# Performance work log

Hardware: AMD Instinct MI355X
Metric: run time of the kernel (lower is better)

## Reference

```python
import jax, jax.numpy as jnp
import numpy as np

B, PS, ENC = 64, 14, 2048
DEC, ATT, EMB = 512, 512, 512
V, L = 10000, 52


def setup_inputs() -> dict:
    key = jax.random.key(0)
    ks = jax.random.split(key, 24)
    rn = lambda k, shp, s=0.02: (jax.random.normal(k, shp) * s).astype(jnp.float32)
    lengths = jax.random.randint(ks[2], (B, 1), 2, L + 1)
    lengths = lengths.at[0, 0].set(L)  # ensure max(decode_lengths) == L-1 (static)
    return {
        "encoder_output": jax.random.normal(ks[0], (B, PS, PS, ENC), jnp.float32),
        "encoded_captions": jax.random.randint(ks[1], (B, L), 0, V),
        "caption_lengths": lengths,
        # embedding (torch init: uniform(-0.1, 0.1))
        "emb_W": jax.random.uniform(ks[3], (V, EMB), jnp.float32, -0.1, 0.1),
        # attention linears
        "att_enc_W": rn(ks[4], (ENC, ATT)), "att_enc_b": jnp.zeros((ATT,), jnp.float32),
        "att_dec_W": rn(ks[5], (DEC, ATT)), "att_dec_b": jnp.zeros((ATT,), jnp.float32),
        "att_full_w": rn(ks[6], (ATT,)), "att_full_b": jnp.zeros((), jnp.float32),
        # LSTMCell(input = EMB + ENC, hidden = DEC)
        "lstm_Wih": rn(ks[7], (4 * DEC, EMB + ENC)), "lstm_Whh": rn(ks[8], (4 * DEC, DEC)),
        "lstm_bih": jnp.zeros((4 * DEC,), jnp.float32), "lstm_bhh": jnp.zeros((4 * DEC,), jnp.float32),
        # init_h / init_c / f_beta / fc
        "initH_W": rn(ks[9], (ENC, DEC)), "initH_b": jnp.zeros((DEC,), jnp.float32),
        "initC_W": rn(ks[10], (ENC, DEC)), "initC_b": jnp.zeros((DEC,), jnp.float32),
        "fbeta_W": rn(ks[11], (DEC, ENC)), "fbeta_b": jnp.zeros((ENC,), jnp.float32),
        "fc_W": jax.random.uniform(ks[12], (DEC, V), jnp.float32, -0.1, 0.1),
        "fc_b": jnp.zeros((V,), jnp.float32),
    }


def reference(encoder_output, encoded_captions, caption_lengths,
              emb_W, att_enc_W, att_enc_b, att_dec_W, att_dec_b,
              att_full_w, att_full_b, lstm_Wih, lstm_Whh, lstm_bih, lstm_bhh,
              initH_W, initH_b, initC_W, initC_b, fbeta_W, fbeta_b, fc_W, fc_b):
    b = encoder_output.shape[0]
    lengths = caption_lengths[:, 0]
    order = jnp.argsort(-lengths)                     # sort descending (sort_idx)
    lengths = lengths[order]
    enc = encoder_output.reshape(b, -1, ENC)[order]   # [B, P, ENC]
    caps = encoded_captions[order]                    # [B, L]
    emb = emb_W[caps]                                 # [B, L, EMB]
    dec_len = lengths - 1                             # decode lengths
    T = caps.shape[1] - 1                             # static max(decode_lengths)

    mean_enc = enc.mean(axis=1)
    h0 = mean_enc @ initH_W + initH_b
    c0 = mean_enc @ initC_W + initC_b
    # precompute encoder half of the attention MLP once
    att1 = jnp.einsum('bpe,ea->bpa', enc, att_enc_W) + att_enc_b  # [B, P, ATT]

    def step(carry, t):
        h, c = carry
        mask = (t < dec_len)[:, None]                 # rows still decoding
        att2 = h @ att_dec_W + att_dec_b              # [B, ATT]
        e = jax.nn.relu(att1 + att2[:, None, :]) @ att_full_w + att_full_b  # [B, P]
        alpha = jax.nn.softmax(e, axis=-1)
        awe = jnp.einsum('bp,bpe->be', alpha, enc)    # attention-weighted encoding
        gate = jax.nn.sigmoid(h @ fbeta_W + fbeta_b)
        x = jnp.concatenate([emb[:, t, :], gate * awe], axis=1)
        gates = x @ lstm_Wih.T + lstm_bih + h @ lstm_Whh.T + lstm_bhh
        i, f, g, o = jnp.split(gates, 4, axis=1)
        c_new = jax.nn.sigmoid(f) * c + jax.nn.sigmoid(i) * jnp.tanh(g)
        h_new = jax.nn.sigmoid(o) * jnp.tanh(c_new)
        pred = h_new @ fc_W + fc_b                    # dropout p=0 -> identity
        h = jnp.where(mask, h_new, h)
        c = jnp.where(mask, c_new, c)
        return (h, c), (jnp.where(mask, pred, 0.0), jnp.where(mask, alpha, 0.0))

    _, (preds, alphas) = jax.lax.scan(step, (h0, c0), jnp.arange(T))
    preds = jnp.transpose(preds, (1, 0, 2))           # [B, T, V]
    alphas = jnp.transpose(alphas, (1, 0, 2))         # [B, T, P]
    return preds, caps, dec_len, alphas, order
```

## Files before the change

kernel.cpp:

```cpp
#include <hip/hip_runtime.h>
#include <hip/hip_cooperative_groups.h>
#include <math.h>

namespace cg = cooperative_groups;

#define BATCH 64
#define PIX   196
#define ENCD  2048
#define DECD  512
#define ATTD  512
#define EMBD  512
#define VOC   10000
#define LCAP  52
#define TSTEPS 51
#define XHDIM 3072

typedef __bf16 bfv8 __attribute__((ext_vector_type(8)));
typedef float  fv4  __attribute__((ext_vector_type(4)));

__device__ __forceinline__ float bf2f(unsigned short u) {
    union { unsigned int i; float f; } x; x.i = ((unsigned int)u) << 16; return x.f;
}
__device__ __forceinline__ unsigned short f2bf(float f) {
    union { float f; unsigned int i; } x; x.f = f;
    unsigned int r = x.i + 0x7fffu + ((x.i >> 16) & 1u);
    return (unsigned short)(r >> 16);
}

__global__ void k_setup(const int* caps, const int* lens,
                        int* order, int* declen,
                        float* caps_out, float* declen_out, float* order_out) {
    __shared__ int sl[64];
    __shared__ int so[64];
    int tid = threadIdx.x;
    sl[tid] = lens[tid];
    __syncthreads();
    int li = sl[tid];
    int pos = 0;
    for (int j = 0; j < 64; ++j) {
        int lj = sl[j];
        if (lj > li || (lj == li && j < tid)) pos++;
    }
    so[pos] = tid;
    __syncthreads();
    int ob = so[tid];
    order[tid] = ob;
    int dl = sl[ob] - 1;
    declen[tid] = dl;
    order_out[tid] = (float)ob;
    declen_out[tid] = (float)dl;
    for (int l = 0; l < LCAP; ++l)
        caps_out[tid * LCAP + l] = (float)caps[ob * LCAP + l];
}

__global__ void k_emb_all(const float* embW, const int* caps, const int* order,
                          unsigned short* emb_all, unsigned short* xh) {
    int b = blockIdx.x, t = blockIdx.y, tid = threadIdx.x;
    int tok = caps[order[b] * LCAP + t];
    float4 v = *(const float4*)(embW + (size_t)tok * EMBD + tid * 4);
    ushort4 o;
    o.x = f2bf(v.x); o.y = f2bf(v.y); o.z = f2bf(v.z); o.w = f2bf(v.w);
    *(ushort4*)(emb_all + ((size_t)t * 64 + b) * EMBD + tid * 4) = o;
    if (t == 0)
        *(ushort4*)(xh + (size_t)b * XHDIM + tid * 4) = o;
}

__global__ __launch_bounds__(256) void k_cvt_T(const float* src, unsigned short* dst,
                                               int R, int C) {
    __shared__ float tile[64][65];
    int c0 = blockIdx.x * 64, r0 = blockIdx.y * 64, tid = threadIdx.x;
    for (int idx = tid; idx < 4096; idx += 256) {
        int r = idx >> 6, c = idx & 63;
        float v = 0.f;
        if (r0 + r < R && c0 + c < C) v = src[(size_t)(r0 + r) * C + c0 + c];
        tile[r][c] = v;
    }
    __syncthreads();
    for (int idx = tid; idx < 4096; idx += 256) {
        int c = idx >> 6, r = idx & 63;
        if (c0 + c < C && r0 + r < R)
            dst[(size_t)(c0 + c) * R + r0 + r] = f2bf(tile[r][c]);
    }
}

__global__ void k_cvt_comb(const float* Wih, const float* Whh, unsigned short* W) {
    int j = blockIdx.x, tid = threadIdx.x;
    int q = j >> 9, d = j & 511;
    int nr = ((d >> 4) << 6) + (q << 4) + (d & 15);
    for (int k = tid * 4; k < XHDIM; k += 1024) {
        const float* src = (k < 2560) ? (Wih + (size_t)j * 2560 + k)
                                      : (Whh + (size_t)j * 512 + (k - 2560));
        float4 v = *(const float4*)src;
        ushort4 o;
        o.x = f2bf(v.x); o.y = f2bf(v.y); o.z = f2bf(v.z); o.w = f2bf(v.w);
        *(ushort4*)(W + (size_t)nr * XHDIM + k) = o;
    }
}

__global__ void k_cvt_enc(const float* enc, const int* order, unsigned short* enc_bf) {
    int b = blockIdx.x, p = blockIdx.y, tid = threadIdx.x;
    const float* src = enc + ((size_t)order[b] * PIX + p) * ENCD + tid * 8;
    float4 v0 = *(const float4*)src;
    float4 v1 = *(const float4*)(src + 4);
    unsigned short o[8];
    o[0] = f2bf(v0.x); o[1] = f2bf(v0.y); o[2] = f2bf(v0.z); o[3] = f2bf(v0.w);
    o[4] = f2bf(v1.x); o[5] = f2bf(v1.y); o[6] = f2bf(v1.z); o[7] = f2bf(v1.w);
    *(uint4*)(enc_bf + ((size_t)b * PIX + p) * ENCD + tid * 8) = *(uint4*)o;
}

__global__ void k_mean(const float* enc, const int* order, float* meanv) {
    int b = blockIdx.x;
    int col = blockIdx.y * 256 + threadIdx.x;
    int ob = order[b];
    const float* base = enc + (size_t)ob * PIX * ENCD + col;
    float acc = 0.f;
    for (int p = 0; p < PIX; ++p) acc += base[(size_t)p * ENCD];
    meanv[b * ENCD + col] = acc * (1.0f / (float)PIX);
}

__global__ __launch_bounds__(256) void k_h0c0(const float* meanv,
                                              const float* WH, const float* bH,
                                              const float* WC, const float* bC,
                                              float* h, float* c, unsigned short* xh) {
    __shared__ float As[64 * 33];
    __shared__ float Bs[32 * 65];
    int nt = blockIdx.x, tid = threadIdx.x;
    const float* W; const float* bias; float* out; int j0; bool isH;
    if (nt < 8) { W = WH; bias = bH; out = h; j0 = nt * 64; isH = true; }
    else        { W = WC; bias = bC; out = c; j0 = (nt - 8) * 64; isH = false; }
    float acc[4][4] = {};
    int tr = tid & 15, tc = tid >> 4;
    for (int k0 = 0; k0 < ENCD; k0 += 32) {
        for (int idx = tid; idx < 512; idx += 256) {
            int rl = idx >> 3, k4 = (idx & 7) << 2;
            float4 v = *(const float4*)(meanv + (size_t)rl * ENCD + k0 + k4);
            float* d = As + rl * 33 + k4;
            d[0] = v.x; d[1] = v.y; d[2] = v.z; d[3] = v.w;
        }
        for (int idx = tid; idx < 512; idx += 256) {
            int k = idx >> 4, j4 = (idx & 15) << 2;
            float4 v = *(const float4*)(W + (size_t)(k0 + k) * DECD + j0 + j4);
            float* d = Bs + k * 65 + j4;
            d[0] = v.x; d[1] = v.y; d[2] = v.z; d[3] = v.w;
        }
        __syncthreads();
        for (int kk = 0; kk < 32; ++kk) {
            float a[4], bb[4];
            for (int i = 0; i < 4; ++i) a[i] = As[(tr * 4 + i) * 33 + kk];
            for (int i = 0; i < 4; ++i) bb[i] = Bs[kk * 65 + tc * 4 + i];
            for (int i = 0; i < 4; ++i)
                for (int j2 = 0; j2 < 4; ++j2) acc[i][j2] += a[i] * bb[j2];
        }
        __syncthreads();
    }
    for (int i = 0; i < 4; ++i)
        for (int j2 = 0; j2 < 4; ++j2) {
            int r = tr * 4 + i, j = j0 + tc * 4 + j2;
            float v = acc[i][j2] + bias[j];
            out[r * DECD + j] = v;
            if (isH) xh[(size_t)r * XHDIM + 2560 + j] = f2bf(v);
        }
}

__device__ __forceinline__ void mm64_core(
    const unsigned short* __restrict__ A, int lda,
    const unsigned short* __restrict__ Bt, int ldb,
    int K, int nvalid,
    unsigned short* __restrict__ As, unsigned short* __restrict__ Bs,
    fv4* __restrict__ acc)
{
    const int tid = threadIdx.x;
    const int lane = tid & 63;
    const int w = tid >> 6, wr = w >> 1, wc = w & 1;
    const int lr = lane & 15, lk = (lane >> 4) << 3;
    const int sr = tid >> 2, sc = (tid & 3) << 3;
    const unsigned short* ap = A + (size_t)sr * lda + sc;
    const unsigned short* bp = Bt + (size_t)sr * ldb + sc;
    const bool bok = sr < nvalid;
    unsigned short* aw = As + sr * 40 + sc;
    unsigned short* bw = Bs + sr * 40 + sc;
    const unsigned short* a0p = As + (wr * 32 + lr) * 40 + lk;
    const unsigned short* a1p = a0p + 16 * 40;
    const unsigned short* b0p = Bs + (wc * 32 + lr) * 40 + lk;
    const unsigned short* b1p = b0p + 16 * 40;

    uint4 av = *(const uint4*)ap;
    uint4 bv;
    if (bok) bv = *(const uint4*)bp; else { bv.x = bv.y = bv.z = bv.w = 0u; }

    for (int k0 = 0; k0 < K; k0 += 32) {
        __syncthreads();
        *(uint4*)aw = av;
        *(uint4*)bw = bv;
        if (k0 + 32 < K) {
            av = *(const uint4*)(ap + k0 + 32);
            if (bok) bv = *(const uint4*)(bp + k0 + 32);
            else { bv.x = bv.y = bv.z = bv.w = 0u; }
        }
        __syncthreads();
        bfv8 a0 = *(const bfv8*)a0p;
        bfv8 a1 = *(const bfv8*)a1p;
        bfv8 b0 = *(const bfv8*)b0p;
        bfv8 b1 = *(const bfv8*)b1p;
        acc[0] = __builtin_amdgcn_mfma_f32_16x16x32_bf16(a0, b0, acc[0], 0, 0, 0);
        acc[1] = __builtin_amdgcn_mfma_f32_16x16x32_bf16(a0, b1, acc[1], 0, 0, 0);
        acc[2] = __builtin_amdgcn_mfma_f32_16x16x32_bf16(a1, b0, acc[2], 0, 0, 0);
        acc[3] = __builtin_amdgcn_mfma_f32_16x16x32_bf16(a1, b1, acc[3], 0, 0, 0);
    }
}

#define MM64_DECL_EPI \
    int lane = threadIdx.x & 63; int w = threadIdx.x >> 6; \
    int wr = w >> 1, wc = w & 1; \
    int rg = (lane >> 4) << 2, cg = lane & 15;

__global__ __launch_bounds__(256) void k_att1_mfma(
    const unsigned short* __restrict__ enc_bf, const unsigned short* __restrict__ WaeT,
    const float* __restrict__ bias, unsigned short* __restrict__ att1bf) {
    __shared__ __align__(16) unsigned short As[64 * 40];
    __shared__ __align__(16) unsigned short Bs[64 * 40];
    int r0 = blockIdx.x * 64, a0 = blockIdx.y * 64;
    fv4 acc[4];
    acc[0] = (fv4)0.f; acc[1] = (fv4)0.f; acc[2] = (fv4)0.f; acc[3] = (fv4)0.f;
    mm64_core(enc_bf + (size_t)r0 * ENCD, ENCD,
              WaeT + (size_t)a0 * ENCD, ENCD, ENCD, 64, As, Bs, acc);
    MM64_DECL_EPI
    #pragma unroll
    for (int m = 0; m < 2; ++m)
      #pragma unroll
      for (int n = 0; n < 2; ++n)
        #pragma unroll
        for (int r = 0; r < 4; ++r) {
            int row = r0 + wr * 32 + m * 16 + rg + r;
            int col = a0 + wc * 32 + n * 16 + cg;
            att1bf[(size_t)row * ATTD + col] = f2bf(acc[m * 2 + n][r] + bias[col]);
        }
}

__device__ __forceinline__ void fc_tile(
    const unsigned short* __restrict__ hallbf, const unsigned short* __restrict__ WfcT,
    const float* __restrict__ bias, const int* __restrict__ declen,
    float* __restrict__ preds, int vt, int tt,
    unsigned short* __restrict__ As, unsigned short* __restrict__ Bs) {
    int v0 = vt * 64;
    int nv = VOC - v0; if (nv > 64) nv = 64;
    fv4 acc[4];
    acc[0] = (fv4)0.f; acc[1] = (fv4)0.f; acc[2] = (fv4)0.f; acc[3] = (fv4)0.f;
    mm64_core(hallbf + (size_t)tt * 64 * DECD, DECD,
              WfcT + (size_t)v0 * DECD, DECD, DECD, nv, As, Bs, acc);
    MM64_DECL_EPI
    #pragma unroll
    for (int m = 0; m < 2; ++m)
      #pragma unroll
      for (int n = 0; n < 2; ++n)
        #pragma unroll
        for (int r = 0; r < 4; ++r) {
            int b = wr * 32 + m * 16 + rg + r;
            int v = v0 + wc * 32 + n * 16 + cg;
            if (v < VOC) {
                bool mask = tt < declen[b];
                preds[((size_t)b * TSTEPS + tt) * VOC + v] =
                    mask ? (acc[m * 2 + n][r] + bias[v]) : 0.f;
            }
        }
}

__global__ __launch_bounds__(256) void k_fc_mfma(
    const unsigned short* __restrict__ hallbf, const unsigned short* __restrict__ WfcT,
    const float* __restrict__ bias, const int* __restrict__ declen,
    float* __restrict__ preds) {
    __shared__ __align__(16) unsigned short As[64 * 40];
    __shared__ __align__(16) unsigned short Bs[64 * 40];
    fc_tile(hallbf, WfcT, bias, declen, preds, blockIdx.x, blockIdx.y, As, Bs);
}

struct LoopArgs {
    const unsigned short* W2T;
    const unsigned short* Wcomb;
    const unsigned short* att1;
    const unsigned short* enc;
    const unsigned short* emb_all;
    const unsigned short* WfcT;
    unsigned short* xh;
    unsigned short* hall;
    const float* bad; const float* bfb;
    const float* wfull; const float* bfull;
    const float* bih; const float* bhh;
    const float* fcb;
    float* att2; float* gate; float* part5;
    float* h; float* c; float* alphas; float* preds;
    const int* declen;
};

__global__ __launch_bounds__(256) void k_loop(LoopArgs a) {
    cg::grid_group grid = cg::this_grid();
    __shared__ __align__(16) unsigned short As[64 * 40];
    __shared__ __align__(16) unsigned short Bs[64 * 40];
    __shared__ float sal[256];
    __shared__ float sred[256];
    __shared__ float sacc[2048];
    __shared__ float gacc[64][65];
    const int bid = blockIdx.x, tid = threadIdx.x;

    for (int t = 0; t < TSTEPS; ++t) {
        if (bid < 40) {
            int j0 = bid * 64;
            fv4 acc[4];
            acc[0] = (fv4)0.f; acc[1] = (fv4)0.f; acc[2] = (fv4)0.f; acc[3] = (fv4)0.f;
            mm64_core(a.xh + 2560, XHDIM, a.W2T + (size_t)j0 * DECD, DECD,
                      DECD, 64, As, Bs, acc);
            MM64_DECL_EPI
            #pragma unroll
            for (int m = 0; m < 2; ++m)
              #pragma unroll
              for (int n = 0; n < 2; ++n)
                #pragma unroll
                for (int r = 0; r < 4; ++r) {
                    int row = wr * 32 + m * 16 + rg + r;
                    int jg = j0 + wc * 32 + n * 16 + cg;
                    float v = acc[m * 2 + n][r];
                    if (jg < ATTD) {
                        a.att2[row * ATTD + jg] = v + a.bad[jg];
                    } else {
                        int jj = jg - ATTD;
                        a.gate[row * ENCD + jj] = 1.f / (1.f + expf(-(v + a.bfb[jj])));
                    }
                }
        } else if (bid < 72) {
            int jt = bid - 40;
            fv4 acc[4];
            acc[0] = (fv4)0.f; acc[1] = (fv4)0.f; acc[2] = (fv4)0.f; acc[3] = (fv4)0.f;
            mm64_core(a.xh + 2560, XHDIM,
                      a.Wcomb + (size_t)jt * 64 * XHDIM + 2560, XHDIM,
                      512, 64, As, Bs, acc);
            MM64_DECL_EPI
            #pragma unroll
            for (int m = 0; m < 2; ++m)
              #pragma unroll
              for (int n = 0; n < 2; ++n)
                #pragma unroll
                for (int r = 0; r < 4; ++r) {
                    int row = wr * 32 + m * 16 + rg + r;
                    int col = jt * 64 + wc * 32 + n * 16 + cg;
                    a.part5[row * 2048 + col] = acc[m * 2 + n][r];
                }
        }
        grid.sync();

        {
            int b = bid >> 2, pair = bid & 3;
            int lane = tid & 63, wv = tid >> 6;
            const float* a2 = a.att2 + b * ATTD + lane * 8;
            float4 a2a = *(const float4*)a2;
            float4 a2b = *(const float4*)(a2 + 4);
            const float* wf = a.wfull + lane * 8;
            float4 wfa = *(const float4*)wf;
            float4 wfb = *(const float4*)(wf + 4);
            float bf0 = a.bfull[0];
            for (int p = wv; p < PIX; p += 4) {
                uint4 v = *(const uint4*)(a.att1 + ((size_t)b * PIX + p) * ATTD + lane * 8);
                const unsigned short* us = (const unsigned short*)&v;
                float accv;
                accv  = fmaxf(bf2f(us[0]) + a2a.x, 0.f) * wfa.x;
                accv += fmaxf(bf2f(us[1]) + a2a.y, 0.f) * wfa.y;
                accv += fmaxf(bf2f(us[2]) + a2a.z, 0.f) * wfa.z;
                accv += fmaxf(bf2f(us[3]) + a2a.w, 0.f) * wfa.w;
                accv += fmaxf(bf2f(us[4]) + a2b.x, 0.f) * wfb.x;
                accv += fmaxf(bf2f(us[5]) + a2b.y, 0.f) * wfb.y;
                accv += fmaxf(bf2f(us[6]) + a2b.z, 0.f) * wfb.z;
                accv += fmaxf(bf2f(us[7]) + a2b.w, 0.f) * wfb.w;
                for (int off = 32; off; off >>= 1) accv += __shfl_down(accv, off);
                if (lane == 0) sacc[p] = accv + bf0;
            }
            __syncthreads();
            float ev = (tid < PIX) ? sacc[tid] : -1e30f;
            sred[tid] = ev; __syncthreads();
            for (int s = 128; s; s >>= 1) {
                if (tid < s) sred[tid] = fmaxf(sred[tid], sred[tid + s]);
                __syncthreads();
            }
            float m = sred[0]; __syncthreads();
            float pv = (tid < PIX) ? expf(ev - m) : 0.f;
            sred[tid] = pv; __syncthreads();
            for (int s = 128; s; s >>= 1) {
                if (tid < s) sred[tid] += sred[tid + s];
                __syncthreads();
            }
            float inv = 1.f / sred[0];
            float al = pv * inv;
            sal[tid] = al;
            if (pair == 0 && tid < PIX) {
                bool mask = t < a.declen[b];
                a.alphas[((size_t)b * TSTEPS + t) * PIX + tid] = mask ? al : 0.f;
            }
            if (tid < 16)
                *(uint4*)(a.xh + (size_t)b * XHDIM + pair * 128 + tid * 8) =
                    *(const uint4*)(a.emb_all + ((size_t)t * 64 + b) * EMBD +
                                    pair * 128 + tid * 8);
            __syncthreads();
            int g = tid & 31, pp = tid >> 5;
            #pragma unroll
            for (int cc = 0; cc < 2; ++cc) {
                int ch = pair * 2 + cc;
                float acc[8] = {};
                const unsigned short* base =
                    a.enc + (size_t)b * PIX * ENCD + ch * 256 + g * 8;
                for (int p = pp; p < PIX; p += 8) {
                    uint4 v = *(const uint4*)(base + (size_t)p * ENCD);
                    const unsigned short* us = (const unsigned short*)&v;
                    float av = sal[p];
                    #pragma unroll
                    for (int jj = 0; jj < 8; ++jj) acc[jj] += av * bf2f(us[jj]);
                }
                #pragma unroll
                for (int jj = 0; jj < 8; ++jj) sacc[pp * 256 + g * 8 + jj] = acc[jj];
                __syncthreads();
                float s = 0.f;
                #pragma unroll
                for (int q = 0; q < 8; ++q) s += sacc[q * 256 + tid];
                int col = ch * 256 + tid;
                a.xh[(size_t)b * XHDIM + EMBD + col] = f2bf(a.gate[b * ENCD + col] * s);
                __syncthreads();
            }
        }
        grid.sync();

        if (bid < 32) {
            int jt = bid;
            fv4 acc[4];
            acc[0] = (fv4)0.f; acc[1] = (fv4)0.f; acc[2] = (fv4)0.f; acc[3] = (fv4)0.f;
            mm64_core(a.xh, XHDIM, a.Wcomb + (size_t)jt * 64 * XHDIM, XHDIM,
                      2560, 64, As, Bs, acc);
            {
                MM64_DECL_EPI
                #pragma unroll
                for (int m = 0; m < 2; ++m)
                  #pragma unroll
                  for (int n = 0; n < 2; ++n)
                    #pragma unroll
                    for (int r = 0; r < 4; ++r)
                        gacc[wr * 32 + m * 16 + rg + r][wc * 32 + n * 16 + cg] =
                            acc[m * 2 + n][r];
            }
            __syncthreads();
            #pragma unroll
            for (int it = 0; it < 4; ++it) {
                int idx = it * 256 + tid;
                int b = idx >> 4, dd = idx & 15;
                int d = jt * 16 + dd;
                float gv[4];
                #pragma unroll
                for (int q = 0; q < 4; ++q) {
                    int ccol = q * 16 + dd;
                    gv[q] = gacc[b][ccol] + a.part5[b * 2048 + jt * 64 + ccol]
                          + a.bih[q * 512 + d] + a.bhh[q * 512 + d];
                }
                float si = 1.f / (1.f + expf(-gv[0]));
                float sf = 1.f / (1.f + expf(-gv[1]));
                float gg = tanhf(gv[2]);
                float so = 1.f / (1.f + expf(-gv[3]));
                float c_old = a.c[b * DECD + d], h_old = a.h[b * DECD + d];
                float c_new = sf * c_old + si * gg;
                float h_new = so * tanhf(c_new);
                bool mask = t < a.declen[b];
                float h_keep = mask ? h_new : h_old;
                a.h[b * DECD + d] = h_keep;
                a.c[b * DECD + d] = mask ? c_new : c_old;
                a.xh[(size_t)b * XHDIM + 2560 + d] = f2bf(h_keep);
                a.hall[((size_t)t * 64 + b) * DECD + d] = f2bf(h_new);
            }
        } else if (bid < 189) {
            if (t > 0)
                fc_tile(a.hall, a.WfcT, a.fcb, a.declen, a.preds,
                        bid - 32, t - 1, As, Bs);
        }
        grid.sync();
    }

    if (bid < 157)
        fc_tile(a.hall, a.WfcT, a.fcb, a.declen, a.preds, bid, TSTEPS - 1, As, Bs);
}

__global__ __launch_bounds__(256) void k_att2gate_mfma(
    const unsigned short* __restrict__ xh, const unsigned short* __restrict__ W2T,
    const float* __restrict__ bad, const float* __restrict__ bfb,
    float* __restrict__ att2, float* __restrict__ gate) {
    __shared__ __align__(16) unsigned short As[64 * 40];
    __shared__ __align__(16) unsigned short Bs[64 * 40];
    int j0 = blockIdx.x * 64;
    fv4 acc[4];
    acc[0] = (fv4)0.f; acc[1] = (fv4)0.f; acc[2] = (fv4)0.f; acc[3] = (fv4)0.f;
    mm64_core(xh + 2560, XHDIM, W2T + (size_t)j0 * DECD, DECD, DECD, 64, As, Bs, acc);
    MM64_DECL_EPI
    for (int m = 0; m < 2; ++m)
      for (int n = 0; n < 2; ++n)
        for (int r = 0; r < 4; ++r) {
            int row = wr * 32 + m * 16 + rg + r;
            int jg = j0 + wc * 32 + n * 16 + cg;
            float v = acc[m * 2 + n][r];
            if (jg < ATTD) att2[row * ATTD + jg] = v + bad[jg];
            else { int jj = jg - ATTD; gate[row * ENCD + jj] = 1.f / (1.f + expf(-(v + bfb[jj]))); }
        }
}

__global__ __launch_bounds__(256) void k_gates_mfma(
    const unsigned short* __restrict__ xh, const unsigned short* __restrict__ W,
    float* __restrict__ partial) {
    __shared__ __align__(16) unsigned short As[64 * 40];
    __shared__ __align__(16) unsigned short Bs[64 * 40];
    int jt = blockIdx.x, kc = blockIdx.y;
    fv4 acc[4];
    acc[0] = (fv4)0.f; acc[1] = (fv4)0.f; acc[2] = (fv4)0.f; acc[3] = (fv4)0.f;
    mm64_core(xh + kc * 512, XHDIM,
              W + (size_t)jt * 64 * XHDIM + kc * 512, XHDIM, 512, 64, As, Bs, acc);
    float* out = partial + (size_t)kc * (64 * 2048);
    MM64_DECL_EPI
    for (int m = 0; m < 2; ++m)
      for (int n = 0; n < 2; ++n)
        for (int r = 0; r < 4; ++r) {
            int row = wr * 32 + m * 16 + rg + r;
            int col = jt * 64 + wc * 32 + n * 16 + cg;
            out[row * 2048 + col] = acc[m * 2 + n][r];
        }
}

__global__ void k_e(const unsigned short* att1bf, const float* att2,
                    const float* wfull, const float* bfull, float* e) {
    __shared__ float a2s[512];
    __shared__ float wfs[512];
    int b = blockIdx.x, tid = threadIdx.x;
    a2s[tid] = att2[b * ATTD + tid];
    a2s[tid + 256] = att2[b * ATTD + tid + 256];
    wfs[tid] = wfull[tid];
    wfs[tid + 256] = wfull[tid + 256];
    __syncthreads();
    int p = blockIdx.y * 4 + (tid >> 6);
    int lane = tid & 63;
    uint4 v = *(const uint4*)(att1bf + ((size_t)b * PIX + p) * ATTD + lane * 8);
    const unsigned short* us = (const unsigned short*)&v;
    float acc = 0.f;
    for (int jj = 0; jj < 8; ++jj) {
        int a = lane * 8 + jj;
        float x = bf2f(us[jj]) + a2s[a];
        x = fmaxf(x, 0.f);
        acc += x * wfs[a];
    }
    for (int off = 32; off; off >>= 1) acc += __shfl_down(acc, off);
    if (lane == 0) e[b * PIX + p] = acc + bfull[0];
}

__global__ void k_awe(const float* e, const unsigned short* enc_bf,
                      const float* gate, const int* declen,
                      unsigned short* xh, float* alphas_out, int t) {
    __shared__ float sal[256];
    __shared__ float sred[256];
    __shared__ float sacc[2048];
    int b = blockIdx.x, ch = blockIdx.y, tid = threadIdx.x;
    float ev = (tid < PIX) ? e[b * PIX + tid] : -1e30f;
    sred[tid] = ev; __syncthreads();
    for (int s = 128; s; s >>= 1) { if (tid < s) sred[tid] = fmaxf(sred[tid], sred[tid + s]); __syncthreads(); }
    float m = sred[0]; __syncthreads();
    float pv = (tid < PIX) ? expf(ev - m) : 0.f;
    sred[tid] = pv; __syncthreads();
    for (int s = 128; s; s >>= 1) { if (tid < s) sred[tid] += sred[tid + s]; __syncthreads(); }
    float inv = 1.f / sred[0];
    float al = pv * inv;
    sal[tid] = al;
    if (ch == 0 && tid < PIX) {
        bool mask = t < declen[b];
        alphas_out[((size_t)b * TSTEPS + t) * PIX + tid] = mask ? al : 0.f;
    }
    __syncthreads();
    int g = tid & 31, pp = tid >> 5;
    float acc[8] = {};
    const unsigned short* base = enc_bf + (size_t)b * PIX * ENCD + ch * 256 + g * 8;
    for (int p = pp; p < PIX; p += 8) {
        uint4 v = *(const uint4*)(base + (size_t)p * ENCD);
        const unsigned short* us = (const unsigned short*)&v;
        float a = sal[p];
        for (int jj = 0; jj < 8; ++jj) acc[jj] += a * bf2f(us[jj]);
    }
    for (int jj = 0; jj < 8; ++jj) sacc[pp * 256 + g * 8 + jj] = acc[jj];
    __syncthreads();
    float s = 0.f;
    for (int q = 0; q < 8; ++q) s += sacc[q * 256 + tid];
    int col = ch * 256 + tid;
    xh[(size_t)b * XHDIM + EMBD + col] = f2bf(gate[b * ENCD + col] * s);
}

__global__ void k_update(const float* partial, const float* bih, const float* bhh,
                         const int* declen, float* h, float* c,
                         unsigned short* hallbf, const unsigned short* emb_all,
                         unsigned short* xh, int t) {
    int b = blockIdx.x, d = threadIdx.x;
    float g[4];
    for (int q = 0; q < 4; ++q) {
        int ncol = ((d >> 4) << 6) + (q << 4) + (d & 15);
        float acc = bih[q * 512 + d] + bhh[q * 512 + d];
        for (int kc = 0; kc < 6; ++kc) acc += partial[(size_t)kc * 131072 + b * 2048 + ncol];
        g[q] = acc;
    }
    float si = 1.f / (1.f + expf(-g[0]));
    float sf = 1.f / (1.f + expf(-g[1]));
    float gg = tanhf(g[2]);
    float so = 1.f / (1.f + expf(-g[3]));
    float c_old = c[b * DECD + d], h_old = h[b * DECD + d];
    float c_new = sf * c_old + si * gg;
    float h_new = so * tanhf(c_new);
    bool mask = t < declen[b];
    float h_keep = mask ? h_new : h_old;
    h[b * DECD + d] = h_keep;
    c[b * DECD + d] = mask ? c_new : c_old;
    xh[(size_t)b * XHDIM + 2560 + d] = f2bf(h_keep);
    hallbf[((size_t)t * 64 + b) * DECD + d] = f2bf(h_new);
    if (t + 1 < TSTEPS)
        xh[(size_t)b * XHDIM + d] = emb_all[((size_t)(t + 1) * 64 + b) * EMBD + d];
}

extern "C" void kernel_launch(void* const* d_in, const int* in_sizes, int n_in,
                              void* d_out, int out_size, void* d_ws, size_t ws_size,
                              hipStream_t stream) {
    const float* enc      = (const float*)d_in[0];
    const int*   caps     = (const int*)d_in[1];
    const int*   lens     = (const int*)d_in[2];
    const float* embW     = (const float*)d_in[3];
    const float* att_enc_W = (const float*)d_in[4];
    const float* att_enc_b = (const float*)d_in[5];
    const float* att_dec_W = (const float*)d_in[6];
    const float* att_dec_b = (const float*)d_in[7];
    const float* att_full_w = (const float*)d_in[8];
    const float* att_full_b = (const float*)d_in[9];
    const float* lstm_Wih = (const float*)d_in[10];
    const float* lstm_Whh = (const float*)d_in[11];
    const float* lstm_bih = (const float*)d_in[12];
    const float* lstm_bhh = (const float*)d_in[13];
    const float* initH_W  = (const float*)d_in[14];
    const float* initH_b  = (const float*)d_in[15];
    const float* initC_W  = (const float*)d_in[16];
    const float* initC_b  = (const float*)d_in[17];
    const float* fbeta_W  = (const float*)d_in[18];
    const float* fbeta_b  = (const float*)d_in[19];
    const float* fc_W     = (const float*)d_in[20];
    const float* fc_b     = (const float*)d_in[21];

    float* o = (float*)d_out;
    float* preds_out  = o;
    float* caps_out   = o + (size_t)BATCH * TSTEPS * VOC;
    float* declen_out = caps_out + (size_t)BATCH * LCAP;
    float* order_out  = declen_out + BATCH;
    float* alphas_out = order_out + BATCH;

    char* wsb = (char*)d_ws;
    int* i_order  = (int*)wsb;
    int* i_declen = i_order + 64;
    float* f = (float*)(wsb + 512);
    float* f_h     = f;  f += (size_t)BATCH * DECD;
    float* f_c     = f;  f += (size_t)BATCH * DECD;
    float* f_att2  = f;  f += (size_t)BATCH * ATTD;
    float* f_gate  = f;  f += (size_t)BATCH * ENCD;
    float* f_e     = f;  f += (size_t)BATCH * PIX;
    f = (float*)(((uintptr_t)f + 255) & ~(uintptr_t)255);
    float* f_part  = f;  f += (size_t)6 * BATCH * 2048;
    float* f_mean = f_part;
    unsigned short* WaeT = (unsigned short*)(f_part + (size_t)BATCH * ENCD);
    f = (float*)(((uintptr_t)f + 255) & ~(uintptr_t)255);
    unsigned short* bf = (unsigned short*)f;
    unsigned short* xh_bf    = bf;  bf += (size_t)BATCH * XHDIM;
    unsigned short* att1_bf  = bf;  bf += (size_t)BATCH * PIX * ATTD;
    unsigned short* Wcomb_bf = bf;  bf += (size_t)2048 * XHDIM;
    unsigned short* W2T      = bf;  bf += (size_t)(ATTD + ENCD) * DECD;
    unsigned short* WfcT     = bf;  bf += (size_t)VOC * DECD;
    unsigned short* emb_all  = bf;  bf += (size_t)TSTEPS * BATCH * EMBD;
    unsigned short* hall_bf  = bf;  bf += (size_t)TSTEPS * BATCH * DECD;
    bf = (unsigned short*)(((uintptr_t)bf + 255) & ~(uintptr_t)255);
    unsigned short* enc_bf   = bf;  bf += (size_t)BATCH * PIX * ENCD;

    k_setup<<<1, 64, 0, stream>>>(caps, lens, i_order, i_declen,
                                  caps_out, declen_out, order_out);
    k_emb_all<<<dim3(BATCH, TSTEPS), 128, 0, stream>>>(embW, caps, i_order,
                                                       emb_all, xh_bf);
    k_cvt_comb<<<2048, 256, 0, stream>>>(lstm_Wih, lstm_Whh, Wcomb_bf);
    k_cvt_enc<<<dim3(BATCH, PIX), 256, 0, stream>>>(enc, i_order, enc_bf);
    k_cvt_T<<<dim3(8, 8),   256, 0, stream>>>(att_dec_W, W2T, DECD, ATTD);
    k_cvt_T<<<dim3(32, 8),  256, 0, stream>>>(fbeta_W, W2T + (size_t)ATTD * DECD, DECD, ENCD);
    k_cvt_T<<<dim3(8, 32),  256, 0, stream>>>(att_enc_W, WaeT, ENCD, ATTD);
    k_cvt_T<<<dim3(157, 8), 256, 0, stream>>>(fc_W, WfcT, DECD, VOC);
    k_mean<<<dim3(BATCH, ENCD / 256), 256, 0, stream>>>(enc, i_order, f_mean);
    k_h0c0<<<16, 256, 0, stream>>>(f_mean, initH_W, initH_b, initC_W, initC_b,
                                   f_h, f_c, xh_bf);
    k_att1_mfma<<<dim3(PIX, ATTD / 64), 256, 0, stream>>>(enc_bf, WaeT,
                                                          att_enc_b, att1_bf);

    int maxb = 0;
    hipError_t qerr = hipOccupancyMaxActiveBlocksPerMultiprocessor(
        &maxb, (const void*)k_loop, 256, 0);
    bool coop_ok = (qerr == hipSuccess) && (maxb >= 1);

    if (coop_ok) {
        LoopArgs la;
        la.W2T = W2T; la.Wcomb = Wcomb_bf; la.att1 = att1_bf; la.enc = enc_bf;
        la.emb_all = emb_all; la.WfcT = WfcT; la.xh = xh_bf; la.hall = hall_bf;
        la.bad = att_dec_b; la.bfb = fbeta_b; la.wfull = att_full_w;
        la.bfull = att_full_b; la.bih = lstm_bih; la.bhh = lstm_bhh;
        la.fcb = fc_b;
        la.att2 = f_att2; la.gate = f_gate; la.part5 = f_part;
        la.h = f_h; la.c = f_c; la.alphas = alphas_out; la.preds = preds_out;
        la.declen = i_declen;
        void* kargs[] = { (void*)&la };
        hipError_t lerr = hipLaunchCooperativeKernel(
            (const void*)k_loop, dim3(256), dim3(256), kargs, 0, stream);
        coop_ok = (lerr == hipSuccess);
    }

    if (!coop_ok) {
        for (int t = 0; t < TSTEPS; ++t) {
            k_att2gate_mfma<<<40, 256, 0, stream>>>(xh_bf, W2T, att_dec_b, fbeta_b,
                                                    f_att2, f_gate);
            k_e<<<dim3(BATCH, 49), 256, 0, stream>>>(att1_bf, f_att2, att_full_w,
                                                     att_full_b, f_e);
            k_awe<<<dim3(BATCH, 8), 256, 0, stream>>>(f_e, enc_bf, f_gate, i_declen,
                                                      xh_bf, alphas_out, t);
            k_gates_mfma<<<dim3(32, 6), 256, 0, stream>>>(xh_bf, Wcomb_bf, f_part);
            k_update<<<BATCH, DECD, 0, stream>>>(f_part, lstm_bih, lstm_bhh, i_declen,
                                                 f_h, f_c, hall_bf, emb_all, xh_bf, t);
        }
        k_fc_mfma<<<dim3((VOC + 63) / 64, TSTEPS), 256, 0, stream>>>(hall_bf, WfcT,
                                                                     fc_b, i_declen,
                                                                     preds_out);
    }
}
```

Baseline: 2.708 ms.

## Rebalance cooperative decode loop work across grid and use MFMA for h0/c0 init

The persistent cooperative loop now uses grid-stride work distribution with up to 512 blocks. The fc projection tiles move into the first phase alongside the att2/gate and h-part GEMMs. The attention score computation is spread over all warps with a global e buffer, which adds an extra grid.sync per step. The softmax/awe stage uses one block per batch-row/octant instead of one per pair. Separately, the init_h/init_c GEMMs switch from an FP32 SIMT kernel to a bf16 MFMA kernel on transposed weights, which costs two extra conversion kernels and some precision.

```diff
diff --git a/kernel.cpp b/kernel.cpp
--- a/kernel.cpp
+++ b/kernel.cpp
@@ -108,58 +108,14 @@
     *(uint4*)(enc_bf + ((size_t)b * PIX + p) * ENCD + tid * 8) = *(uint4*)o;
 }
 
-__global__ void k_mean(const float* enc, const int* order, float* meanv) {
+__global__ void k_mean(const float* enc, const int* order, unsigned short* mean_bf) {
     int b = blockIdx.x;
     int col = blockIdx.y * 256 + threadIdx.x;
     int ob = order[b];
     const float* base = enc + (size_t)ob * PIX * ENCD + col;
     float acc = 0.f;
     for (int p = 0; p < PIX; ++p) acc += base[(size_t)p * ENCD];
-    meanv[b * ENCD + col] = acc * (1.0f / (float)PIX);
-}
-
-__global__ __launch_bounds__(256) void k_h0c0(const float* meanv,
-                                              const float* WH, const float* bH,
-                                              const float* WC, const float* bC,
-                                              float* h, float* c, unsigned short* xh) {
-    __shared__ float As[64 * 33];
-    __shared__ float Bs[32 * 65];
-    int nt = blockIdx.x, tid = threadIdx.x;
-    const float* W; const float* bias; float* out; int j0; bool isH;
-    if (nt < 8) { W = WH; bias = bH; out = h; j0 = nt * 64; isH = true; }
-    else        { W = WC; bias = bC; out = c; j0 = (nt - 8) * 64; isH = false; }
-    float acc[4][4] = {};
-    int tr = tid & 15, tc = tid >> 4;
-    for (int k0 = 0; k0 < ENCD; k0 += 32) {
-        for (int idx = tid; idx < 512; idx += 256) {
-            int rl = idx >> 3, k4 = (idx & 7) << 2;
-            float4 v = *(const float4*)(meanv + (size_t)rl * ENCD + k0 + k4);
-            float* d = As + rl * 33 + k4;
-            d[0] = v.x; d[1] = v.y; d[2] = v.z; d[3] = v.w;
-        }
-        for (int idx = tid; idx < 512; idx += 256) {
-            int k = idx >> 4, j4 = (idx & 15) << 2;
-            float4 v = *(const float4*)(W + (size_t)(k0 + k) * DECD + j0 + j4);
-            float* d = Bs + k * 65 + j4;
-            d[0] = v.x; d[1] = v.y; d[2] = v.z; d[3] = v.w;
-        }
-        __syncthreads();
-        for (int kk = 0; kk < 32; ++kk) {
-            float a[4], bb[4];
-            for (int i = 0; i < 4; ++i) a[i] = As[(tr * 4 + i) * 33 + kk];
-            for (int i = 0; i < 4; ++i) bb[i] = Bs[kk * 65 + tc * 4 + i];
-            for (int i = 0; i < 4; ++i)
-                for (int j2 = 0; j2 < 4; ++j2) acc[i][j2] += a[i] * bb[j2];
-        }
-        __syncthreads();
-    }
-    for (int i = 0; i < 4; ++i)
-        for (int j2 = 0; j2 < 4; ++j2) {
-            int r = tr * 4 + i, j = j0 + tc * 4 + j2;
-            float v = acc[i][j2] + bias[j];
-            out[r * DECD + j] = v;
-            if (isH) xh[(size_t)r * XHDIM + 2560 + j] = f2bf(v);
-        }
+    mean_bf[b * ENCD + col] = f2bf(acc * (1.0f / (float)PIX));
 }
 
 __device__ __forceinline__ void mm64_core(
@@ -213,6 +169,38 @@
     int lane = threadIdx.x & 63; int w = threadIdx.x >> 6; \
     int wr = w >> 1, wc = w & 1; \
     int rg = (lane >> 4) << 2, cg = lane & 15;
+
+__global__ __launch_bounds__(256) void k_h0c0_mfma(
+    const unsigned short* __restrict__ mean_bf,
+    const unsigned short* __restrict__ WinT,
+    const unsigned short* __restrict__ WicT,
+    const float* __restrict__ bH, const float* __restrict__ bC,
+    float* __restrict__ h, float* __restrict__ c, unsigned short* __restrict__ xh) {
+    __shared__ __align__(16) unsigned short As[64 * 40];
+    __shared__ __align__(16) unsigned short Bs[64 * 40];
+    int nt = blockIdx.x;
+    bool isH = nt < 8;
+    int j0 = (nt & 7) * 64;
+    const unsigned short* Bt = (isH ? WinT : WicT) + (size_t)j0 * ENCD;
+    const float* bias = isH ? bH : bC;
+    float* out = isH ? h : c;
+    fv4 acc[4];
+    acc[0] = (fv4)0.f; acc[1] = (fv4)0.f; acc[2] = (fv4)0.f; acc[3] = (fv4)0.f;
+    mm64_core(mean_bf, ENCD, Bt, ENCD, ENCD, 64, As, Bs, acc);
+    MM64_DECL_EPI
+    #pragma unroll
+    for (int m = 0; m < 2; ++m)
+      #pragma unroll
+      for (int n = 0; n < 2; ++n)
+        #pragma unroll
+        for (int r = 0; r < 4; ++r) {
+            int row = wr * 32 + m * 16 + rg + r;
+            int j = j0 + wc * 32 + n * 16 + cg;
+            float v = acc[m * 2 + n][r] + bias[j];
+            out[row * DECD + j] = v;
+            if (isH) xh[(size_t)row * XHDIM + 2560 + j] = f2bf(v);
+        }
+}
 
 __global__ __launch_bounds__(256) void k_att1_mfma(
     const unsigned short* __restrict__ enc_bf, const unsigned short* __restrict__ WaeT,
@@ -287,7 +275,7 @@
     const float* wfull; const float* bfull;
     const float* bih; const float* bhh;
     const float* fcb;
-    float* att2; float* gate; float* part5;
+    float* att2; float* gate; float* e; float* part5;
     float* h; float* c; float* alphas; float* preds;
     const int* declen;
 };
@@ -296,70 +284,77 @@
     cg::grid_group grid = cg::this_grid();
     __shared__ __align__(16) unsigned short As[64 * 40];
     __shared__ __align__(16) unsigned short Bs[64 * 40];
+    __shared__ float sred[256];
     __shared__ float sal[256];
-    __shared__ float sred[256];
-    __shared__ float sacc[2048];
+    __shared__ float sacc[8][256];
     __shared__ float gacc[64][65];
     const int bid = blockIdx.x, tid = threadIdx.x;
+    const int NB = gridDim.x;
 
     for (int t = 0; t < TSTEPS; ++t) {
-        if (bid < 40) {
-            int j0 = bid * 64;
-            fv4 acc[4];
-            acc[0] = (fv4)0.f; acc[1] = (fv4)0.f; acc[2] = (fv4)0.f; acc[3] = (fv4)0.f;
-            mm64_core(a.xh + 2560, XHDIM, a.W2T + (size_t)j0 * DECD, DECD,
-                      DECD, 64, As, Bs, acc);
-            MM64_DECL_EPI
-            #pragma unroll
-            for (int m = 0; m < 2; ++m)
-              #pragma unroll
-              for (int n = 0; n < 2; ++n)
+        for (int it = bid; it < 229; it += NB) {
+            if (it < 40) {
+                int j0 = it * 64;
+                fv4 acc[4];
+                acc[0] = (fv4)0.f; acc[1] = (fv4)0.f; acc[2] = (fv4)0.f; acc[3] = (fv4)0.f;
+                mm64_core(a.xh + 2560, XHDIM, a.W2T + (size_t)j0 * DECD, DECD,
+                          DECD, 64, As, Bs, acc);
+                MM64_DECL_EPI
                 #pragma unroll
-                for (int r = 0; r < 4; ++r) {
-                    int row = wr * 32 + m * 16 + rg + r;
-                    int jg = j0 + wc * 32 + n * 16 + cg;
-                    float v = acc[m * 2 + n][r];
-                    if (jg < ATTD) {
-                        a.att2[row * ATTD + jg] = v + a.bad[jg];
-                    } else {
-                        int jj = jg - ATTD;
-                        a.gate[row * ENCD + jj] = 1.f / (1.f + expf(-(v + a.bfb[jj])));
+                for (int m = 0; m < 2; ++m)
+                  #pragma unroll
+                  for (int n = 0; n < 2; ++n)
+                    #pragma unroll
+                    for (int r = 0; r < 4; ++r) {
+                        int row = wr * 32 + m * 16 + rg + r;
+                        int jg = j0 + wc * 32 + n * 16 + cg;
+                        float v = acc[m * 2 + n][r];
+                        if (jg < ATTD) {
+                            a.att2[row * ATTD + jg] = v + a.bad[jg];
+                        } else {
+                            int jj = jg - ATTD;
+                            a.gate[row * ENCD + jj] = 1.f / (1.f + expf(-(v + a.bfb[jj])));
+                        }
                     }
-                }
-        } else if (bid < 72) {
-            int jt = bid - 40;
-            fv4 acc[4];
-            acc[0] = (fv4)0.f; acc[1] = (fv4)0.f; acc[2] = (fv4)0.f; acc[3] = (fv4)0.f;
-            mm64_core(a.xh + 2560, XHDIM,
-                      a.Wcomb + (size_t)jt * 64 * XHDIM + 2560, XHDIM,
-                      512, 64, As, Bs, acc);
-            MM64_DECL_EPI
-            #pragma unroll
-            for (int m = 0; m < 2; ++m)
-              #pragma unroll
-              for (int n = 0; n < 2; ++n)
+            } else if (it < 72) {
+                int jt = it - 40;
+                fv4 acc[4];
+                acc[0] = (fv4)0.f; acc[1] = (fv4)0.f; acc[2] = (fv4)0.f; acc[3] = (fv4)0.f;
+                mm64_core(a.xh + 2560, XHDIM,
+                          a.Wcomb + (size_t)jt * 64 * XHDIM + 2560, XHDIM,
+                          512, 64, As, Bs, acc);
+                MM64_DECL_EPI
                 #pragma unroll
-                for (int r = 0; r < 4; ++r) {
-                    int row = wr * 32 + m * 16 + rg + r;
-                    int col = jt * 64 + wc * 32 + n * 16 + cg;
-                    a.part5[row * 2048 + col] = acc[m * 2 + n][r];
-                }
+                for (int m = 0; m < 2; ++m)
+                  #pragma unroll
+                  for (int n = 0; n < 2; ++n)
+                    #pragma unroll
+                    for (int r = 0; r < 4; ++r) {
+                        int row = wr * 32 + m * 16 + rg + r;
+                        int col = jt * 64 + wc * 32 + n * 16 + cg;
+                        a.part5[row * 2048 + col] = acc[m * 2 + n][r];
+                    }
+            } else if (t > 0) {
+                fc_tile(a.hall, a.WfcT, a.fcb, a.declen, a.preds,
+                        it - 72, t - 1, As, Bs);
+            }
         }
         grid.sync();
 
         {
-            int b = bid >> 2, pair = bid & 3;
-            int lane = tid & 63, wv = tid >> 6;
-            const float* a2 = a.att2 + b * ATTD + lane * 8;
-            float4 a2a = *(const float4*)a2;
-            float4 a2b = *(const float4*)(a2 + 4);
-            const float* wf = a.wfull + lane * 8;
-            float4 wfa = *(const float4*)wf;
-            float4 wfb = *(const float4*)(wf + 4);
-            float bf0 = a.bfull[0];
-            for (int p = wv; p < PIX; p += 4) {
+            int lane = tid & 63;
+            int gw = bid * 4 + (tid >> 6);
+            const int stride = NB * 4;
+            for (int u = gw; u < BATCH * PIX; u += stride) {
+                int b = u / PIX, p = u % PIX;
                 uint4 v = *(const uint4*)(a.att1 + ((size_t)b * PIX + p) * ATTD + lane * 8);
                 const unsigned short* us = (const unsigned short*)&v;
+                const float* a2 = a.att2 + b * ATTD + lane * 8;
+                float4 a2a = *(const float4*)a2;
+                float4 a2b = *(const float4*)(a2 + 4);
+                const float* wf = a.wfull + lane * 8;
+                float4 wfa = *(const float4*)wf;
+                float4 wfb = *(const float4*)(wf + 4);
                 float accv;
                 accv  = fmaxf(bf2f(us[0]) + a2a.x, 0.f) * wfa.x;
                 accv += fmaxf(bf2f(us[1]) + a2a.y, 0.f) * wfa.y;
@@ -370,10 +365,15 @@
                 accv += fmaxf(bf2f(us[6]) + a2b.z, 0.f) * wfb.z;
                 accv += fmaxf(bf2f(us[7]) + a2b.w, 0.f) * wfb.w;
                 for (int off = 32; off; off >>= 1) accv += __shfl_down(accv, off);
-                if (lane == 0) sacc[p] = accv + bf0;
-            }
+                if (lane == 0) a.e[u] = accv + a.bfull[0];
+            }
+        }
+        grid.sync();
+
+        for (int it = bid; it < 512; it += NB) {
             __syncthreads();
-            float ev = (tid < PIX) ? sacc[tid] : -1e30f;
+            int b = it >> 3, oct = it & 7;
+            float ev = (tid < PIX) ? a.e[b * PIX + tid] : -1e30f;
             sred[tid] = ev; __syncthreads();
             for (int s = 128; s; s >>= 1) {
                 if (tid < s) sred[tid] = fmaxf(sred[tid], sred[tid + s]);
@@ -389,44 +389,38 @@
             float inv = 1.f / sred[0];
             float al = pv * inv;
             sal[tid] = al;
-            if (pair == 0 && tid < PIX) {
+            if (oct == 0 && tid < PIX) {
                 bool mask = t < a.declen[b];
                 a.alphas[((size_t)b * TSTEPS + t) * PIX + tid] = mask ? al : 0.f;
             }
-            if (tid < 16)
-                *(uint4*)(a.xh + (size_t)b * XHDIM + pair * 128 + tid * 8) =
-                    *(const uint4*)(a.emb_all + ((size_t)t * 64 + b) * EMBD +
-                                    pair * 128 + tid * 8);
+            if (oct == 0 && tid < 64)
+                *(uint4*)(a.xh + (size_t)b * XHDIM + tid * 8) =
+                    *(const uint4*)(a.emb_all + ((size_t)t * 64 + b) * EMBD + tid * 8);
             __syncthreads();
             int g = tid & 31, pp = tid >> 5;
+            float acc[8] = {};
+            const unsigned short* base =
+                a.enc + (size_t)b * PIX * ENCD + oct * 256 + g * 8;
+            for (int p = pp; p < PIX; p += 8) {
+                uint4 v = *(const uint4*)(base + (size_t)p * ENCD);
+                const unsigned short* us = (const unsigned short*)&v;
+                float av = sal[p];
+                #pragma unroll
+                for (int jj = 0; jj < 8; ++jj) acc[jj] += av * bf2f(us[jj]);
+            }
             #pragma unroll
-            for (int cc = 0; cc < 2; ++cc) {
-                int ch = pair * 2 + cc;
-                float acc[8] = {};
-                const unsigned short* base =
-                    a.enc + (size_t)b * PIX * ENCD + ch * 256 + g * 8;
-                for (int p = pp; p < PIX; p += 8) {
-                    uint4 v = *(const uint4*)(base + (size_t)p * ENCD);
-                    const unsigned short* us = (const unsigned short*)&v;
-                    float av = sal[p];
-                    #pragma unroll
-                    for (int jj = 0; jj < 8; ++jj) acc[jj] += av * bf2f(us[jj]);
-                }
-                #pragma unroll
-                for (int jj = 0; jj < 8; ++jj) sacc[pp * 256 + g * 8 + jj] = acc[jj];
-                __syncthreads();
-                float s = 0.f;
-                #pragma unroll
-                for (int q = 0; q < 8; ++q) s += sacc[q * 256 + tid];
-                int col = ch * 256 + tid;
-                a.xh[(size_t)b * XHDIM + EMBD + col] = f2bf(a.gate[b * ENCD + col] * s);
-                __syncthreads();
-            }
+            for (int jj = 0; jj < 8; ++jj) sacc[pp][g * 8 + jj] = acc[jj];
+            __syncthreads();
+            float s = 0.f;
+            #pragma unroll
+            for (int q = 0; q < 8; ++q) s += sacc[q][tid];
+            int col = oct * 256 + tid;
+            a.xh[(size_t)b * XHDIM + EMBD + col] = f2bf(a.gate[b * ENCD + col] * s);
         }
         grid.sync();
 
-        if (bid < 32) {
-            int jt = bid;
+        for (int it = bid; it < 32; it += NB) {
+            int jt = it;
             fv4 acc[4];
             acc[0] = (fv4)0.f; acc[1] = (fv4)0.f; acc[2] = (fv4)0.f; acc[3] = (fv4)0.f;
             mm64_core(a.xh, XHDIM, a.Wcomb + (size_t)jt * 64 * XHDIM, XHDIM,
@@ -444,8 +438,8 @@
             }
             __syncthreads();
             #pragma unroll
-            for (int it = 0; it < 4; ++it) {
-                int idx = it * 256 + tid;
+            for (int i4 = 0; i4 < 4; ++i4) {
+                int idx = i4 * 256 + tid;
                 int b = idx >> 4, dd = idx & 15;
                 int d = jt * 16 + dd;
                 float gv[4];
@@ -469,16 +463,13 @@
                 a.xh[(size_t)b * XHDIM + 2560 + d] = f2bf(h_keep);
                 a.hall[((size_t)t * 64 + b) * DECD + d] = f2bf(h_new);
             }
-        } else if (bid < 189) {
-            if (t > 0)
-                fc_tile(a.hall, a.WfcT, a.fcb, a.declen, a.preds,
-                        bid - 32, t - 1, As, Bs);
+            __syncthreads();
         }
         grid.sync();
     }
 
-    if (bid < 157)
-        fc_tile(a.hall, a.WfcT, a.fcb, a.declen, a.preds, bid, TSTEPS - 1, As, Bs);
+    for (int it = bid; it < 157; it += NB)
+        fc_tile(a.hall, a.WfcT, a.fcb, a.declen, a.preds, it, TSTEPS - 1, As, Bs);
 }
 
 __global__ __launch_bounds__(256) void k_att2gate_mfma(
@@ -661,7 +652,7 @@
     float* f_e     = f;  f += (size_t)BATCH * PIX;
     f = (float*)(((uintptr_t)f + 255) & ~(uintptr_t)255);
     float* f_part  = f;  f += (size_t)6 * BATCH * 2048;
-    float* f_mean = f_part;
+    unsigned short* mean_bf = (unsigned short*)f_part;
     unsigned short* WaeT = (unsigned short*)(f_part + (size_t)BATCH * ENCD);
     f = (float*)(((uintptr_t)f + 255) & ~(uintptr_t)255);
     unsigned short* bf = (unsigned short*)f;
@@ -672,6 +663,8 @@
     unsigned short* WfcT     = bf;  bf += (size_t)VOC * DECD;
     unsigned short* emb_all  = bf;  bf += (size_t)TSTEPS * BATCH * EMBD;
     unsigned short* hall_bf  = bf;  bf += (size_t)TSTEPS * BATCH * DECD;
+    unsigned short* WinT     = bf;  bf += (size_t)DECD * ENCD;
+    unsigned short* WicT     = bf;  bf += (size_t)DECD * ENCD;
     bf = (unsigned short*)(((uintptr_t)bf + 255) & ~(uintptr_t)255);
     unsigned short* enc_bf   = bf;  bf += (size_t)BATCH * PIX * ENCD;
 
@@ -685,9 +678,11 @@
     k_cvt_T<<<dim3(32, 8),  256, 0, stream>>>(fbeta_W, W2T + (size_t)ATTD * DECD, DECD, ENCD);
     k_cvt_T<<<dim3(8, 32),  256, 0, stream>>>(att_enc_W, WaeT, ENCD, ATTD);
     k_cvt_T<<<dim3(157, 8), 256, 0, stream>>>(fc_W, WfcT, DECD, VOC);
-    k_mean<<<dim3(BATCH, ENCD / 256), 256, 0, stream>>>(enc, i_order, f_mean);
-    k_h0c0<<<16, 256, 0, stream>>>(f_mean, initH_W, initH_b, initC_W, initC_b,
-                                   f_h, f_c, xh_bf);
+    k_cvt_T<<<dim3(8, 32),  256, 0, stream>>>(initH_W, WinT, ENCD, DECD);
+    k_cvt_T<<<dim3(8, 32),  256, 0, stream>>>(initC_W, WicT, ENCD, DECD);
+    k_mean<<<dim3(BATCH, ENCD / 256), 256, 0, stream>>>(enc, i_order, mean_bf);
+    k_h0c0_mfma<<<16, 256, 0, stream>>>(mean_bf, WinT, WicT, initH_b, initC_b,
+                                        f_h, f_c, xh_bf);
     k_att1_mfma<<<dim3(PIX, ATTD / 64), 256, 0, stream>>>(enc_bf, WaeT,
                                                           att_enc_b, att1_bf);
 
@@ -695,6 +690,7 @@
     hipError_t qerr = hipOccupancyMaxActiveBlocksPerMultiprocessor(
         &maxb, (const void*)k_loop, 256, 0);
     bool coop_ok = (qerr == hipSuccess) && (maxb >= 1);
+    int NB = (maxb >= 2) ? 512 : 256;
 
     if (coop_ok) {
         LoopArgs la;
@@ -703,12 +699,12 @@
         la.bad = att_dec_b; la.bfb = fbeta_b; la.wfull = att_full_w;
         la.bfull = att_full_b; la.bih = lstm_bih; la.bhh = lstm_bhh;
         la.fcb = fc_b;
-        la.att2 = f_att2; la.gate = f_gate; la.part5 = f_part;
+        la.att2 = f_att2; la.gate = f_gate; la.e = f_e; la.part5 = f_part;
         la.h = f_h; la.c = f_c; la.alphas = alphas_out; la.preds = preds_out;
         la.declen = i_declen;
         void* kargs[] = { (void*)&la };
         hipError_t lerr = hipLaunchCooperativeKernel(
-            (const void*)k_loop, dim3(256), dim3(256), kargs, 0, stream);
+            (const void*)k_loop, dim3(NB), dim3(256), kargs, 0, stream);
         coop_ok = (lerr == hipSuccess);
     }
 
```

Result: slower. 9.674 ms (+257.2%).
